# Kernel optimization log

Hardware: AMD Instinct MI355X
Metric: run time of the kernel (lower is better)

The kernel has to match this reference:

```python
import jax, jax.numpy as jnp
import numpy as np

LN_EPS = 1e-9

def _layer_norm(x, g, b):
    mu = jnp.mean(x, axis=-1, keepdims=True)
    var = jnp.mean((x - mu) ** 2, axis=-1, keepdims=True)
    return (x - mu) * jax.lax.rsqrt(var + LN_EPS) * g + b

def _ffn(x, w1, b1, w2, b2, ln_g, ln_b):
    h = jax.nn.gelu(x @ w1 + b1, approximate=False)
    h = h @ w2 + b2
    return _layer_norm(h, ln_g, ln_b)

def _kernel_mean(x, y):
    d = x.shape[1]
    x2 = jnp.sum(x * x, axis=1)[:, None]
    y2 = jnp.sum(y * y, axis=1)[None, :]
    sq = x2 + y2 - 2.0 * (x @ y.T)  # [Nx, Ny]
    return jnp.mean(jnp.exp(-sq / (d * d)))

def _mmd(x, y):
    return _kernel_mean(x, x) + _kernel_mean(y, y) - 2.0 * _kernel_mean(x, y)

def setup_inputs() -> dict:
    key = jax.random.key(0)
    ks = jax.random.split(key, 8)
    B, S, D, DI, DL = 8, 512, 1024, 4096, 64
    s = lambda fan: 1.0 / np.sqrt(fan)
    return {
        "hidden": jax.random.normal(ks[0], (B, S, D), jnp.float32),
        "true_samples": jax.random.normal(ks[1], (B * S, DL), jnp.float32),
        "enc_w1": jax.random.normal(ks[2], (D, DI), jnp.float32) * s(D),
        "enc_b1": jnp.zeros((DI,), jnp.float32),
        "enc_w2": jax.random.normal(ks[3], (DI, DL), jnp.float32) * s(DI),
        "enc_b2": jnp.zeros((DL,), jnp.float32),
        "enc_ln_g": jnp.ones((DL,), jnp.float32),
        "enc_ln_b": jnp.zeros((DL,), jnp.float32),
        "dec_w1": jax.random.normal(ks[4], (DL, DI), jnp.float32) * s(DL),
        "dec_b1": jnp.zeros((DI,), jnp.float32),
        "dec_w2": jax.random.normal(ks[5], (DI, D), jnp.float32) * s(DI),
        "dec_b2": jnp.zeros((D,), jnp.float32),
        "dec_ln_g": jnp.ones((D,), jnp.float32),
        "dec_ln_b": jnp.zeros((D,), jnp.float32),
    }

def reference(hidden, true_samples, enc_w1, enc_b1, enc_w2, enc_b2, enc_ln_g, enc_ln_b,
              dec_w1, dec_b1, dec_w2, dec_b2, dec_ln_g, dec_ln_b):
    latent = _ffn(hidden, enc_w1, enc_b1, enc_w2, enc_b2, enc_ln_g, enc_ln_b)  # [B,S,DL]
    recon = _ffn(latent, dec_w1, dec_b1, dec_w2, dec_b2, dec_ln_g, dec_ln_b)   # [B,S,D]
    B, S, DL = latent.shape
    lat_flat = latent.reshape(-1, DL)  # [B*S, DL]
    reg_loss = _mmd(true_samples, lat_flat) / B * S
    return recon, latent, reg_loss
```

## Files before the change

kernel.cpp:

```cpp
#include <hip/hip_runtime.h>
#include <hip/hip_bf16.h>
#include <math.h>


typedef __attribute__((ext_vector_type(8))) short short8;
typedef __attribute__((ext_vector_type(4))) float float4a;
typedef __attribute__((ext_vector_type(4))) unsigned short us4;

__device__ inline ushort bf16r(float x) {
    union { float f; unsigned u; } c; c.f = x;
    unsigned r = (c.u + 0x7fffu + ((c.u >> 16) & 1u)) >> 16;
    return (ushort)r;
}

__device__ inline void gld_lds16(const void* g, void* l) {
    __builtin_amdgcn_global_load_lds(
        (const __attribute__((address_space(1))) void*)g,
        (__attribute__((address_space(3))) void*)l, 16, 0, 0);
}

__device__ inline float fast_gelu(float v) {
    float v2 = v * v;
    float u = v * __builtin_fmaf(0.07135481627f, v2, 1.5957691216f);
    u = fminf(u, 30.0f);
    float e = __expf(u);
    return v * e * __builtin_amdgcn_rcpf(e + 1.0f);
}

__global__ __launch_bounds__(256) void k_pre(
        const float* __restrict__ hidden, ushort* __restrict__ A1bf,
        const float* __restrict__ tsamp, ushort* __restrict__ Tbf,
        float* __restrict__ sq_t, float* __restrict__ acc,
        const float* __restrict__ i0, ushort* __restrict__ o0,
        const float* __restrict__ i1, ushort* __restrict__ o1,
        const float* __restrict__ i2, ushort* __restrict__ o2,
        const float* __restrict__ i3, ushort* __restrict__ o3) {
    int b = blockIdx.x, tid = threadIdx.x;
    if (b == 0 && tid < 24) acc[tid] = 0.0f;
    if (b < 4096) {
        int i = b * 1024 + tid * 4;
        float4 v = *(const float4*)(hidden + i);
        us4 o = {bf16r(v.x), bf16r(v.y), bf16r(v.z), bf16r(v.w)};
        *(us4*)(A1bf + i) = o;
        return;
    }
    if (b < 4352) {
        int i = (b - 4096) * 1024 + tid * 4;
        float4 v = *(const float4*)(tsamp + i);
        us4 o = {bf16r(v.x), bf16r(v.y), bf16r(v.z), bf16r(v.w)};
        *(us4*)(Tbf + i) = o;
        float s = v.x * v.x + v.y * v.y + v.z * v.z + v.w * v.w;
#pragma unroll
        for (int off = 8; off; off >>= 1) s += __shfl_xor(s, off);
        if ((tid & 15) == 0) sq_t[i >> 6] = s;
        return;
    }
    __shared__ float t[32][33];
    const float* in; ushort* out; int R, C, lb;
    if (b < 8448)      { in = i0; out = o0; R = 1024; C = 4096; lb = b - 4352; }
    else if (b < 8704) { in = i1; out = o1; R = 4096; C = 64;   lb = b - 8448; }
    else if (b < 8960) { in = i2; out = o2; R = 64;   C = 4096; lb = b - 8704; }
    else               { in = i3; out = o3; R = 4096; C = 1024; lb = b - 8960; }
    int bx = (lb % (C / 32)) * 32;
    int by = (lb / (C / 32)) * 32;
    int tx = tid & 31, ty = tid >> 5;
#pragma unroll
    for (int i = 0; i < 32; i += 8)
        t[ty + i][tx] = in[(size_t)(by + ty + i) * C + (bx + tx)];
    __syncthreads();
#pragma unroll
    for (int i = 0; i < 32; i += 8)
        out[(size_t)(bx + ty + i) * R + (by + tx)] = bf16r(t[tx][ty + i]);
}

template <int BN, int EPI, bool SWZ>
__global__ __launch_bounds__(256) void k_gemm(
        const ushort* __restrict__ A, const ushort* __restrict__ Bt,
        const float* __restrict__ bias, void* __restrict__ Out,
        float* __restrict__ Out2, int M, int N, int K, int KC) {
    constexpr int BM = 128, BK = 64;
    constexpr int WAVES_N = BN / 64;
    constexpr int WAVES_M = 4 / WAVES_N;
    constexpr int WM = BM / WAVES_M;
    constexpr int MT = WM / 16;
    constexpr int NT = 4;
    constexpr int CA = BM / 32, CB = BN / 32;

    __shared__ ushort sA[BM * 64];
    __shared__ ushort sB[BN * 64];

    const int tid  = threadIdx.x;
    const int wave = tid >> 6, lane = tid & 63;
    const int wm = wave / WAVES_N, wn = wave % WAVES_N;
    int bx = blockIdx.x, by = blockIdx.y;
    if constexpr (SWZ) {
        int lin = blockIdx.x + gridDim.x * blockIdx.y;
        by = lin % gridDim.y;
        bx = lin / gridDim.y;
    }
    const int m0 = by * BM, n0 = bx * BN;
    const int lrow = lane & 15, lq = lane >> 4;
    const int srow8 = lane >> 3;
    const int sk8   = lane & 7;
    const int kbeg = blockIdx.z * KC;

    const ushort* pA[CA]; unsigned lA[CA];
#pragma unroll
    for (int j = 0; j < CA; ++j) {
        int c = wave * CA + j;
        int r = c * 8 + srow8;
        pA[j] = &A[(size_t)(m0 + r) * K + kbeg + ((sk8 ^ (r & 7)) * 8)];
        lA[j] = c * 512;
    }
    const ushort* pB[CB]; unsigned lB[CB];
#pragma unroll
    for (int j = 0; j < CB; ++j) {
        int c = wave * CB + j;
        int r = c * 8 + srow8;
        pB[j] = &Bt[(size_t)(n0 + r) * K + kbeg + ((sk8 ^ (r & 7)) * 8)];
        lB[j] = c * 512;
    }
    unsigned aoff[2][MT], boff[2][NT];
#pragma unroll
    for (int h = 0; h < 2; ++h) {
#pragma unroll
        for (int mt = 0; mt < MT; ++mt) {
            int r = wm * WM + mt * 16 + lrow;
            aoff[h][mt] = r * 64 + (((h * 4 + lq) ^ (r & 7)) * 8);
        }
#pragma unroll
        for (int nt = 0; nt < NT; ++nt) {
            int r = wn * 64 + nt * 16 + lrow;
            boff[h][nt] = r * 64 + (((h * 4 + lq) ^ (r & 7)) * 8);
        }
    }

    float4a acc[MT][NT];
#pragma unroll
    for (int mt = 0; mt < MT; ++mt)
#pragma unroll
        for (int nt = 0; nt < NT; ++nt)
            acc[mt][nt] = (float4a){0.f, 0.f, 0.f, 0.f};

    for (int k0 = 0; k0 < KC; k0 += BK) {
#pragma unroll
        for (int j = 0; j < CA; ++j) {
            gld_lds16(pA[j], &sA[lA[j]]);
            pA[j] += BK;
        }
#pragma unroll
        for (int j = 0; j < CB; ++j) {
            gld_lds16(pB[j], &sB[lB[j]]);
            pB[j] += BK;
        }
        __syncthreads();
#pragma unroll
        for (int h = 0; h < 2; ++h) {
            short8 af[MT], bfr[NT];
#pragma unroll
            for (int mt = 0; mt < MT; ++mt)
                af[mt] = *(short8*)(&sA[aoff[h][mt]]);
#pragma unroll
            for (int nt = 0; nt < NT; ++nt)
                bfr[nt] = *(short8*)(&sB[boff[h][nt]]);
#pragma unroll
            for (int mt = 0; mt < MT; ++mt)
#pragma unroll
                for (int nt = 0; nt < NT; ++nt)
                    acc[mt][nt] = __builtin_amdgcn_mfma_f32_16x16x32_bf16(
                        af[mt], bfr[nt], acc[mt][nt], 0, 0, 0);
        }
        __syncthreads();
    }

    float* dstp = nullptr;
    if constexpr (EPI == 2) {
        if (Out2 && blockIdx.z) dstp = Out2;
        else dstp = (float*)Out + (size_t)blockIdx.z * M * N;
    }
#pragma unroll
    for (int mt = 0; mt < MT; ++mt)
#pragma unroll
        for (int nt = 0; nt < NT; ++nt) {
            int col = n0 + wn * 64 + nt * 16 + lrow;
            float bv = 0.f;
            if constexpr (EPI != 2) bv = bias[col];
#pragma unroll
            for (int r = 0; r < 4; ++r) {
                int row = m0 + wm * WM + mt * 16 + lq * 4 + r;
                float v = acc[mt][nt][r] + bv;
                if constexpr (EPI == 0) {
                    ((ushort*)Out)[(size_t)row * N + col] = bf16r(fast_gelu(v));
                } else if constexpr (EPI == 1) {
                    ((float*)Out)[(size_t)row * N + col] = v;
                } else {
                    dstp[(size_t)row * N + col] = v;
                }
            }
        }
}

__global__ __launch_bounds__(256) void k_gram_all(
        const ushort* __restrict__ Tbf, const ushort* __restrict__ Lbf,
        const float* __restrict__ sq_t, const float* __restrict__ sq_l,
        float* __restrict__ accum) {
    __shared__ ushort sX[128 * 64];
    __shared__ ushort sY[128 * 64];
    __shared__ float red[4];

    int id = blockIdx.x;
    int pair, tbx, tby; float w;
    if (id < 1056) {
        pair = (id < 528) ? 0 : 1;
        int t = (pair == 0) ? id : id - 528;
        int r = (int)((sqrtf(8.0f * t + 1.0f) - 1.0f) * 0.5f);
        while ((r + 1) * (r + 2) / 2 <= t) ++r;
        while (r * (r + 1) / 2 > t) --r;
        tby = r; tbx = t - r * (r + 1) / 2;
        w = (tbx == tby) ? 1.0f : 2.0f;
    } else {
        pair = 2; int t = id - 1056;
        tbx = t & 31; tby = t >> 5; w = 1.0f;
    }
    const ushort* Xb = (pair == 1) ? Lbf : Tbf;
    const ushort* Yb = (pair == 0) ? Tbf : Lbf;
    const float* sqX = (pair == 1) ? sq_l : sq_t;
    const float* sqY = (pair == 0) ? sq_t : sq_l;

    const int tid  = threadIdx.x;
    const int wave = tid >> 6, lane = tid & 63;
    const int wm = wave >> 1, wn = wave & 1;
    const int bx = tbx * 128, by = tby * 128;
    const int lrow = lane & 15, lq = lane >> 4;
    const int srow8 = lane >> 3, sk8 = lane & 7;

#pragma unroll
    for (int j = 0; j < 4; ++j) {
        int c = wave * 4 + j;
        int r = c * 8 + srow8;
        int kc = (sk8 ^ (r & 7)) * 8;
        gld_lds16(&Xb[(size_t)(bx + r) * 64 + kc], &sX[c * 512]);
        gld_lds16(&Yb[(size_t)(by + r) * 64 + kc], &sY[c * 512]);
    }

    unsigned xoff[2][4], yoff[2][4];
#pragma unroll
    for (int h = 0; h < 2; ++h)
#pragma unroll
        for (int i = 0; i < 4; ++i) {
            int rx = wm * 64 + i * 16 + lrow;
            int ry = wn * 64 + i * 16 + lrow;
            xoff[h][i] = rx * 64 + (((h * 4 + lq) ^ (rx & 7)) * 8);
            yoff[h][i] = ry * 64 + (((h * 4 + lq) ^ (ry & 7)) * 8);
        }
    __syncthreads();

    float4a acc[4][4];
#pragma unroll
    for (int mt = 0; mt < 4; ++mt)
#pragma unroll
        for (int nt = 0; nt < 4; ++nt)
            acc[mt][nt] = (float4a){0.f, 0.f, 0.f, 0.f};

#pragma unroll
    for (int h = 0; h < 2; ++h) {
        short8 xf[4], yf[4];
#pragma unroll
        for (int mt = 0; mt < 4; ++mt)
            xf[mt] = *(short8*)(&sX[xoff[h][mt]]);
#pragma unroll
        for (int nt = 0; nt < 4; ++nt)
            yf[nt] = *(short8*)(&sY[yoff[h][nt]]);
#pragma unroll
        for (int mt = 0; mt < 4; ++mt)
#pragma unroll
            for (int nt = 0; nt < 4; ++nt)
                acc[mt][nt] = __builtin_amdgcn_mfma_f32_16x16x32_bf16(
                    xf[mt], yf[nt], acc[mt][nt], 0, 0, 0);
    }

    float sy[4];
#pragma unroll
    for (int nt = 0; nt < 4; ++nt)
        sy[nt] = sqY[by + wn * 64 + nt * 16 + lrow];
    float s = 0.f;
#pragma unroll
    for (int mt = 0; mt < 4; ++mt)
#pragma unroll
        for (int r = 0; r < 4; ++r) {
            float sx = sqX[bx + wm * 64 + mt * 16 + lq * 4 + r];
#pragma unroll
            for (int nt = 0; nt < 4; ++nt)
                s += __expf((2.0f * acc[mt][nt][r] - sx - sy[nt]) * (1.0f / 4096.0f));
        }
    s *= w;
#pragma unroll
    for (int off = 32; off; off >>= 1) s += __shfl_xor(s, off);
    if ((tid & 63) == 0) red[tid >> 6] = s;
    __syncthreads();
    if (tid == 0) atomicAdd(accum + pair * 8, red[0] + red[1] + red[2] + red[3]);
}

__global__ __launch_bounds__(256) void k_ln64_red(
        const float* __restrict__ part, int npart,
        const float* __restrict__ bias, const float* __restrict__ g,
        const float* __restrict__ b, float* __restrict__ outf,
        ushort* __restrict__ outb, float* __restrict__ sq_l) {
    int wave = threadIdx.x >> 6, lane = threadIdx.x & 63;
    int row = blockIdx.x * 4 + wave;
    float x = bias[lane];
    for (int s = 0; s < npart; ++s)
        x += part[(size_t)s * 4096 * 64 + row * 64 + lane];
    float s = x;
#pragma unroll
    for (int off = 32; off; off >>= 1) s += __shfl_xor(s, off);
    float mu = s * (1.0f / 64.0f);
    float d = x - mu;
    float v = d * d;
#pragma unroll
    for (int off = 32; off; off >>= 1) v += __shfl_xor(v, off);
    float rs = rsqrtf(v * (1.0f / 64.0f) + 1e-9f);
    float y = d * rs * g[lane] + b[lane];
    outf[row * 64 + lane] = y;
    outb[row * 64 + lane] = bf16r(y);
    float q = y * y;
#pragma unroll
    for (int off = 32; off; off >>= 1) q += __shfl_xor(q, off);
    if (lane == 0) sq_l[row] = q;
}

__global__ __launch_bounds__(256) void k_ln1024_red(
        const float* __restrict__ p0, const float* __restrict__ p1,
        const float* __restrict__ bias, const float* __restrict__ g,
        const float* __restrict__ b, float* __restrict__ out) {
    __shared__ float red[4];
    int row = blockIdx.x, tid = threadIdx.x;
    const float4 v0 = *(const float4*)(p0 + (size_t)row * 1024 + tid * 4);
    const float4 v1 = *(const float4*)(p1 + (size_t)row * 1024 + tid * 4);
    const float4 bb = *(const float4*)(bias + tid * 4);
    float4 v;
    v.x = v0.x + v1.x + bb.x;
    v.y = v0.y + v1.y + bb.y;
    v.z = v0.z + v1.z + bb.z;
    v.w = v0.w + v1.w + bb.w;
    float s = v.x + v.y + v.z + v.w;
#pragma unroll
    for (int off = 32; off; off >>= 1) s += __shfl_xor(s, off);
    if ((tid & 63) == 0) red[tid >> 6] = s;
    __syncthreads();
    float mu = (red[0] + red[1] + red[2] + red[3]) * (1.0f / 1024.0f);
    float dx = v.x - mu, dy = v.y - mu, dz = v.z - mu, dw = v.w - mu;
    float q = dx * dx + dy * dy + dz * dz + dw * dw;
#pragma unroll
    for (int off = 32; off; off >>= 1) q += __shfl_xor(q, off);
    __syncthreads();
    if ((tid & 63) == 0) red[tid >> 6] = q;
    __syncthreads();
    float rs = rsqrtf((red[0] + red[1] + red[2] + red[3]) * (1.0f / 1024.0f) + 1e-9f);
    const float4 gv = *(const float4*)(g + tid * 4);
    const float4 bv = *(const float4*)(b + tid * 4);
    float4 o;
    o.x = dx * rs * gv.x + bv.x;
    o.y = dy * rs * gv.y + bv.y;
    o.z = dz * rs * gv.z + bv.z;
    o.w = dw * rs * gv.w + bv.w;
    *(float4*)(out + (size_t)row * 1024 + tid * 4) = o;
}

__global__ void k_finalize(const float* __restrict__ accum, float* __restrict__ out) {
    out[0] = (accum[0] + accum[8] - 2.0f * accum[16]) * (64.0f / (4096.0f * 4096.0f));
}

extern "C" void kernel_launch(void* const* d_in, const int* in_sizes, int n_in,
                              void* d_out, int out_size, void* d_ws, size_t ws_size,
                              hipStream_t stream) {
    const float* hidden   = (const float*)d_in[0];
    const float* tsamp    = (const float*)d_in[1];
    const float* enc_w1   = (const float*)d_in[2];
    const float* enc_b1   = (const float*)d_in[3];
    const float* enc_w2   = (const float*)d_in[4];
    const float* enc_b2   = (const float*)d_in[5];
    const float* enc_ln_g = (const float*)d_in[6];
    const float* enc_ln_b = (const float*)d_in[7];
    const float* dec_w1   = (const float*)d_in[8];
    const float* dec_b1   = (const float*)d_in[9];
    const float* dec_w2   = (const float*)d_in[10];
    const float* dec_b2   = (const float*)d_in[11];
    const float* dec_ln_g = (const float*)d_in[12];
    const float* dec_ln_b = (const float*)d_in[13];

    float* out      = (float*)d_out;
    float* recon    = out;
    float* latent_f = out + 4194304;
    float* reg      = out + 4456448;

    char* ws = (char*)d_ws;
    const size_t MB = 1024 * 1024;
    ushort* A1bf = (ushort*)(ws + 0);
    ushort* W1t  = (ushort*)(ws + 8 * MB);
    float*  part = (float*)(ws + 0);
    float*  h4p0 = (float*)(ws + 0);
    ushort* H1bf = (ushort*)(ws + 16 * MB);
    ushort* W4t  = (ushort*)(ws + 48 * MB);
    ushort* W2t  = (ushort*)(ws + 56 * MB);
    ushort* W3t  = (ushort*)(ws + 56 * MB + 512 * 1024);
    ushort* Lbf  = (ushort*)(ws + 57 * MB);
    float*  sq_t = (float*)(ws + 59 * MB);
    float*  sq_l = (float*)(ws + 59 * MB + 16384);
    float*  acc3 = (float*)(ws + 59 * MB + 32768);
    ushort* Tbf  = (ushort*)(ws + 59 * MB + 65536);

    k_pre<<<13056, 256, 0, stream>>>(hidden, A1bf, tsamp, Tbf, sq_t, acc3,
                                     enc_w1, W1t, enc_w2, W2t,
                                     dec_w1, W3t, dec_w2, W4t);

    k_gemm<64, 0, false><<<dim3(64, 32, 1), 256, 0, stream>>>(
        A1bf, W1t, enc_b1, H1bf, nullptr, 4096, 4096, 1024, 1024);
    k_gemm<64, 2, false><<<dim3(1, 32, 16), 256, 0, stream>>>(
        H1bf, W2t, nullptr, part, nullptr, 4096, 64, 4096, 256);
    k_ln64_red<<<1024, 256, 0, stream>>>(part, 16, enc_b2, enc_ln_g, enc_ln_b,
                                         latent_f, Lbf, sq_l);

    k_gemm<64, 0, false><<<dim3(64, 32, 1), 256, 0, stream>>>(
        Lbf, W3t, dec_b1, H1bf, nullptr, 4096, 4096, 64, 64);
    k_gemm<64, 2, true><<<dim3(16, 32, 2), 256, 0, stream>>>(
        H1bf, W4t, nullptr, h4p0, recon, 4096, 1024, 4096, 2048);
    k_ln1024_red<<<4096, 256, 0, stream>>>(h4p0, recon, dec_b2, dec_ln_g,
                                           dec_ln_b, recon);

    k_gram_all<<<2080, 256, 0, stream>>>(Tbf, Lbf, sq_t, sq_l, acc3);
    k_finalize<<<1, 1, 0, stream>>>(acc3, reg);
}
```

Before: 273.2 us.

## Add 256-row tiled GEMM kernel with 512 threads and deeper prefetch for large GEMMs

Result: slower. 283.7 us (+3.9%).

```diff
diff --git a/kernel.cpp b/kernel.cpp
--- a/kernel.cpp
+++ b/kernel.cpp
@@ -17,6 +17,12 @@
     __builtin_amdgcn_global_load_lds(
         (const __attribute__((address_space(1))) void*)g,
         (__attribute__((address_space(3))) void*)l, 16, 0, 0);
+}
+
+template <int N> __device__ inline void wait_vmcnt() {
+    if constexpr (N == 0) asm volatile("s_waitcnt vmcnt(0)" ::: "memory");
+    else if constexpr (N == 4) asm volatile("s_waitcnt vmcnt(4)" ::: "memory");
+    else if constexpr (N == 6) asm volatile("s_waitcnt vmcnt(6)" ::: "memory");
 }
 
 __device__ inline float fast_gelu(float v) {
@@ -196,6 +202,163 @@
                 } else {
                     dstp[(size_t)row * N + col] = v;
                 }
+            }
+        }
+}
+
+template <int BN, int EPI>
+__global__ __launch_bounds__(512, 2) void k_gemm256(
+        const ushort* __restrict__ A, const ushort* __restrict__ Bt,
+        const float* __restrict__ bias, void* __restrict__ Out,
+        float* __restrict__ Out2, int M, int N, int K, int KC) {
+    constexpr int BM = 256, BK = 64;
+    constexpr int AI = 4;
+    constexpr int BI = BN / 64;
+    constexpr int BLO = (BN == 256) ? 2 : 0;
+    constexpr int WAVES_N = BN / 64;
+    constexpr int WAVES_M = 8 / WAVES_N;
+    constexpr int WM = BM / WAVES_M;
+    constexpr int MT = WM / 16;
+    constexpr int NT = 4;
+    constexpr int PH = MT / 2;
+    constexpr int INF = AI + BLO;
+
+    __shared__ ushort sA[2][BM * 64];
+    __shared__ ushort sB[2][BN * 64];
+
+    const int tid = threadIdx.x;
+    const int wave = tid >> 6, lane = tid & 63;
+    const int wm = wave / WAVES_N, wn = wave % WAVES_N;
+    const int m0 = blockIdx.y * BM, n0 = blockIdx.x * BN;
+    const int lrow = lane & 15, lq = lane >> 4;
+    const int kbeg = blockIdx.z * KC;
+    const int nT = KC / BK;
+
+    const int crow = tid >> 3;
+    const int ck8  = (tid & 7) ^ (crow & 7);
+    const ushort* pAbase = A  + (size_t)(m0 + crow) * K + kbeg + ck8 * 8;
+    const ushort* pBbase = Bt + (size_t)(n0 + crow) * K + kbeg + ck8 * 8;
+
+    const int a0  = (wm * WM + lrow) * 64;
+    const int b0  = (wn * 64 + lrow) * 64;
+    const int sw0 = ((lq) ^ (lrow & 7)) * 8;
+    const int sw1 = ((4 + lq) ^ (lrow & 7)) * 8;
+
+    float4a acc[MT][NT];
+#pragma unroll
+    for (int mt = 0; mt < MT; ++mt)
+#pragma unroll
+        for (int nt = 0; nt < NT; ++nt)
+            acc[mt][nt] = (float4a){0.f, 0.f, 0.f, 0.f};
+
+#pragma unroll
+    for (int j = 0; j < AI; ++j)
+        gld_lds16(pAbase + (size_t)j * 64 * K, &sA[0][j * 4096 + wave * 512]);
+#pragma unroll
+    for (int j = 0; j < BI; ++j)
+        gld_lds16(pBbase + (size_t)j * 64 * K, &sB[0][j * 4096 + wave * 512]);
+    if (nT > 1) {
+#pragma unroll
+        for (int j = 0; j < AI; ++j)
+            gld_lds16(pAbase + (size_t)j * 64 * K + BK,
+                      &sA[1][j * 4096 + wave * 512]);
+#pragma unroll
+        for (int j = 0; j < BLO; ++j)
+            gld_lds16(pBbase + (size_t)j * 64 * K + BK,
+                      &sB[1][j * 4096 + wave * 512]);
+        wait_vmcnt<INF>();
+    } else {
+        wait_vmcnt<0>();
+    }
+    __builtin_amdgcn_s_barrier();
+    __builtin_amdgcn_sched_barrier(0);
+
+    short8 bfr[2][NT];
+
+    for (int t = 0; t < nT; ++t) {
+        const int d = t & 1;
+        const bool pf1 = (t + 1 < nT), pf2 = (t + 2 < nT);
+        const size_t koff1 = (size_t)(t + 1) * BK;
+        const size_t koff2 = (size_t)(t + 2) * BK;
+
+#pragma unroll
+        for (int q = 0; q < PH; ++q) {
+            short8 af[2][2];
+#pragma unroll
+            for (int i = 0; i < 2; ++i) {
+                af[0][i] = *(const short8*)(&sA[d][a0 + (q * 2 + i) * 1024 + sw0]);
+                af[1][i] = *(const short8*)(&sA[d][a0 + (q * 2 + i) * 1024 + sw1]);
+            }
+            if (q == 0) {
+#pragma unroll
+                for (int nt = 0; nt < NT; ++nt) {
+                    bfr[0][nt] = *(const short8*)(&sB[d][b0 + nt * 1024 + sw0]);
+                    bfr[1][nt] = *(const short8*)(&sB[d][b0 + nt * 1024 + sw1]);
+                }
+                if (pf1) {
+#pragma unroll
+                    for (int j = BLO; j < BLO + 2; ++j)
+                        gld_lds16(pBbase + (size_t)j * 64 * K + koff1,
+                                  &sB[d ^ 1][j * 4096 + wave * 512]);
+                }
+            }
+            __builtin_amdgcn_s_barrier();
+            asm volatile("s_waitcnt lgkmcnt(0)" ::: "memory");
+            __builtin_amdgcn_sched_barrier(0);
+            __builtin_amdgcn_s_setprio(1);
+#pragma unroll
+            for (int h = 0; h < 2; ++h)
+#pragma unroll
+                for (int i = 0; i < 2; ++i)
+#pragma unroll
+                    for (int nt = 0; nt < NT; ++nt)
+                        acc[q * 2 + i][nt] =
+                            __builtin_amdgcn_mfma_f32_16x16x32_bf16(
+                                af[h][i], bfr[h][nt], acc[q * 2 + i][nt],
+                                0, 0, 0);
+            __builtin_amdgcn_s_setprio(0);
+            __builtin_amdgcn_sched_barrier(0);
+            __builtin_amdgcn_s_barrier();
+            __builtin_amdgcn_sched_barrier(0);
+        }
+        if (pf2) {
+#pragma unroll
+            for (int j = 0; j < AI; ++j)
+                gld_lds16(pAbase + (size_t)j * 64 * K + koff2,
+                          &sA[d][j * 4096 + wave * 512]);
+#pragma unroll
+            for (int j = 0; j < BLO; ++j)
+                gld_lds16(pBbase + (size_t)j * 64 * K + koff2,
+                          &sB[d][j * 4096 + wave * 512]);
+        }
+        if (pf1) {
+            if (pf2) wait_vmcnt<INF>();
+            else     wait_vmcnt<0>();
+            __builtin_amdgcn_s_barrier();
+            __builtin_amdgcn_sched_barrier(0);
+        }
+    }
+
+    float* dstp = nullptr;
+    if constexpr (EPI == 2) {
+        if (Out2 && blockIdx.z) dstp = Out2;
+        else dstp = (float*)Out + (size_t)blockIdx.z * M * N;
+    }
+#pragma unroll
+    for (int mt = 0; mt < MT; ++mt)
+#pragma unroll
+        for (int nt = 0; nt < NT; ++nt) {
+            const int col = n0 + wn * 64 + nt * 16 + lrow;
+            float bv = 0.f;
+            if constexpr (EPI == 0) bv = bias[col];
+#pragma unroll
+            for (int r = 0; r < 4; ++r) {
+                const int row = m0 + wm * WM + mt * 16 + lq * 4 + r;
+                float v = acc[mt][nt][r] + bv;
+                if constexpr (EPI == 0)
+                    ((ushort*)Out)[(size_t)row * N + col] = bf16r(fast_gelu(v));
+                else
+                    dstp[(size_t)row * N + col] = v;
             }
         }
 }
@@ -414,7 +577,7 @@
                                      enc_w1, W1t, enc_w2, W2t,
                                      dec_w1, W3t, dec_w2, W4t);
 
-    k_gemm<64, 0, false><<<dim3(64, 32, 1), 256, 0, stream>>>(
+    k_gemm256<256, 0><<<dim3(16, 16, 1), 512, 0, stream>>>(
         A1bf, W1t, enc_b1, H1bf, nullptr, 4096, 4096, 1024, 1024);
     k_gemm<64, 2, false><<<dim3(1, 32, 16), 256, 0, stream>>>(
         H1bf, W2t, nullptr, part, nullptr, 4096, 64, 4096, 256);
@@ -423,7 +586,7 @@
 
     k_gemm<64, 0, false><<<dim3(64, 32, 1), 256, 0, stream>>>(
         Lbf, W3t, dec_b1, H1bf, nullptr, 4096, 4096, 64, 64);
-    k_gemm<64, 2, true><<<dim3(16, 32, 2), 256, 0, stream>>>(
+    k_gemm256<128, 2><<<dim3(8, 16, 2), 512, 0, stream>>>(
         H1bf, W4t, nullptr, h4p0, recon, 4096, 1024, 4096, 2048);
     k_ln1024_red<<<4096, 256, 0, stream>>>(h4p0, recon, dec_b2, dec_ln_g,
                                            dec_ln_b, recon);
```
